# Optimization experiments

Hardware: AMD Instinct MI355X
Metric: run time of the kernel (lower is better)

Reference implementation:

```python
import jax, jax.numpy as jnp
import numpy as np

T, B = 100, 256
NUM_IN, NUM_HID, NUM_OUT = 784, 512, 10
BETA = 0.95
THRESH = 1.0   # snntorch Leaky default threshold
SLOPE = 25.0   # surrogate.fast_sigmoid default slope

# Heaviside spike with fast_sigmoid surrogate gradient (snntorch semantics)
@jax.custom_vjp
def spike_fn(x):
    return (x > 0).astype(x.dtype)

def _spike_fwd(x):
    return spike_fn(x), x

def _spike_bwd(x, g):
    return (g / (SLOPE * jnp.abs(x) + 1.0) ** 2,)

spike_fn.defvjp(_spike_fwd, _spike_bwd)

def setup_inputs() -> dict:
    key = jax.random.key(0)
    ks = jax.random.split(key, 5)
    x = jax.random.normal(ks[0], (T, B, NUM_IN), dtype=jnp.float32)
    w1 = jax.random.normal(ks[1], (NUM_HID, NUM_IN), dtype=jnp.float32) / np.float32(np.sqrt(NUM_IN))
    b1 = jax.random.normal(ks[2], (NUM_HID,), dtype=jnp.float32) * 0.01
    w2 = jax.random.normal(ks[3], (NUM_OUT, NUM_HID), dtype=jnp.float32) / np.float32(np.sqrt(NUM_HID))
    b2 = jax.random.normal(ks[4], (NUM_OUT,), dtype=jnp.float32) * 0.01
    return {"x": x, "w1": w1, "b1": b1, "w2": w2, "b2": b2}

def _snn_forward(x, w1, b1, w2, b2):
    mem1_0 = jnp.zeros((B, NUM_HID), x.dtype)
    mem2_0 = jnp.zeros((B, NUM_OUT), x.dtype)

    def step(carry, xt):
        mem1, mem2 = carry
        # layer 1: Linear + Leaky (reset-by-subtraction, reset detached as in snntorch)
        cur1 = xt @ w1.T + b1
        reset1 = jax.lax.stop_gradient(spike_fn(mem1 - THRESH))
        mem1 = BETA * mem1 + cur1 - reset1 * THRESH
        spk1 = spike_fn(mem1 - THRESH)
        # layer 2
        cur2 = spk1 @ w2.T + b2
        reset2 = jax.lax.stop_gradient(spike_fn(mem2 - THRESH))
        mem2 = BETA * mem2 + cur2 - reset2 * THRESH
        spk2 = spike_fn(mem2 - THRESH)
        return (mem1, mem2), (cur2, spk2, spk1, mem2, mem1)

    _, ys = jax.lax.scan(step, (mem1_0, mem2_0), x)
    # ys = (cur_list, spk_list, spk_hidden_list, mem_list, mem_hidden_list), stacked over T
    return ys

def reference(x, w1, b1, w2, b2):
    return _snn_forward(x, w1, b1, w2, b2)
```

## Files before the change

### kernel.cpp

```cpp
#include <hip/hip_runtime.h>
#include <stdint.h>

#define T_STEPS 100
#define BATCH   256
#define NIN     784
#define NHID    512
#define NOUT    10


#define BM 128
#define BN 128
#define BK 8
#define PANEL_K 384

__global__ __launch_bounds__(256) void gemm1_dual(
    const float* __restrict__ X, const float* __restrict__ W,
    float* __restrict__ C1, float* __restrict__ C2)
{
    __shared__ float As[2][BK][BM + 4];
    __shared__ float Bs[2][BK][BN + 4];

    const int tid = threadIdx.x;
    const int bm  = blockIdx.x * BM;
    const int bn  = blockIdx.y * BN;
    const int kb  = blockIdx.z ? PANEL_K : 0;
    float* __restrict__ C = blockIdx.z ? C2 : C1;

    const int row  = tid >> 1;
    const int koff = (tid & 1) * 4;

    const int w    = tid >> 6;
    const int lane = tid & 63;
    const int tm   = (w & 1) * 64 + (lane & 7) * 8;
    const int tn   = (w >> 1) * 64 + (lane >> 3) * 8;

    float acc[8][8];
    #pragma unroll
    for (int i = 0; i < 8; ++i)
        #pragma unroll
        for (int j = 0; j < 8; ++j) acc[i][j] = 0.f;

    const float* Xp = X + (size_t)(bm + row) * NIN + kb + koff;
    const float* Wp = W + (size_t)(bn + row) * NIN + kb + koff;

    float4 pa = *(const float4*)(Xp);
    float4 pb = *(const float4*)(Wp);
    As[0][koff+0][row] = pa.x; As[0][koff+1][row] = pa.y;
    As[0][koff+2][row] = pa.z; As[0][koff+3][row] = pa.w;
    Bs[0][koff+0][row] = pb.x; Bs[0][koff+1][row] = pb.y;
    Bs[0][koff+2][row] = pb.z; Bs[0][koff+3][row] = pb.w;

    const int NITER = PANEL_K / BK;
    for (int it = 0; it < NITER; ++it) {
        const int cur = it & 1;
        __syncthreads();

        if (it + 1 < NITER) {
            const int k0 = (it + 1) * BK;
            pa = *(const float4*)(Xp + k0);
            pb = *(const float4*)(Wp + k0);
        }

        #pragma unroll
        for (int kk = 0; kk < BK; ++kk) {
            float4 av0 = *(const float4*)&As[cur][kk][tm];
            float4 av1 = *(const float4*)&As[cur][kk][tm + 4];
            float4 bv0 = *(const float4*)&Bs[cur][kk][tn];
            float4 bv1 = *(const float4*)&Bs[cur][kk][tn + 4];
            float a[8] = {av0.x, av0.y, av0.z, av0.w, av1.x, av1.y, av1.z, av1.w};
            float b[8] = {bv0.x, bv0.y, bv0.z, bv0.w, bv1.x, bv1.y, bv1.z, bv1.w};
            #pragma unroll
            for (int i = 0; i < 8; ++i)
                #pragma unroll
                for (int j = 0; j < 8; ++j)
                    acc[i][j] = fmaf(a[i], b[j], acc[i][j]);
        }

        if (it + 1 < NITER) {
            const int nxt = cur ^ 1;
            As[nxt][koff+0][row] = pa.x; As[nxt][koff+1][row] = pa.y;
            As[nxt][koff+2][row] = pa.z; As[nxt][koff+3][row] = pa.w;
            Bs[nxt][koff+0][row] = pb.x; Bs[nxt][koff+1][row] = pb.y;
            Bs[nxt][koff+2][row] = pb.z; Bs[nxt][koff+3][row] = pb.w;
        }
    }

    #pragma unroll
    for (int i = 0; i < 8; ++i) {
        size_t r = (size_t)(bm + tm + i) * NHID + bn + tn;
        *(float4*)&C[r]     = make_float4(acc[i][0], acc[i][1], acc[i][2], acc[i][3]);
        *(float4*)&C[r + 4] = make_float4(acc[i][4], acc[i][5], acc[i][6], acc[i][7]);
    }
}

__global__ __launch_bounds__(1024) void leaky_hidden_fused(
    float* __restrict__ mem_io,
    const float* c2,
    float* spk_out,
    const float* __restrict__ X,
    const float* __restrict__ W1,
    const float* __restrict__ b1)
{
    __shared__ float4 xs4[T_STEPS][4];
    __shared__ float  p1s[2][8][NHID];
    __shared__ float  p2s[2][8][NHID];

    const int tid = threadIdx.x;
    const int bb  = blockIdx.x;
    const size_t STRIDE = (size_t)BATCH * NHID;
    const size_t base   = (size_t)bb * NHID;

    if (tid < T_STEPS * 4) {
        const int t = tid >> 2, q = tid & 3;
        xs4[t][q] = *(const float4*)(X + (size_t)t * BATCH * NIN
                                       + (size_t)bb * NIN + 768 + q * 4);
    }

    const bool producer = (tid >= 512);
    const int  lane     = tid & 511;
    const size_t col    = base + lane;

    float wt[16];
    float bias = 0.f;
    float mem  = 0.f;

    if (producer) {
        float v1[8], v2[8];
        #pragma unroll
        for (int j = 0; j < 8; ++j) {
            v1[j] = mem_io[col + (size_t)j * STRIDE];
            v2[j] = c2[col + (size_t)j * STRIDE];
        }
        #pragma unroll
        for (int j = 0; j < 8; ++j) {
            p1s[0][j][lane] = v1[j];
            p2s[0][j][lane] = v2[j];
        }
    } else {
        const int h = lane;
        const float* wp = W1 + (size_t)h * NIN + 768;
        float4 w0  = *(const float4*)(wp);
        float4 w1v = *(const float4*)(wp + 4);
        float4 w2v = *(const float4*)(wp + 8);
        float4 w3v = *(const float4*)(wp + 12);
        wt[0]=w0.x;  wt[1]=w0.y;  wt[2]=w0.z;  wt[3]=w0.w;
        wt[4]=w1v.x; wt[5]=w1v.y; wt[6]=w1v.z; wt[7]=w1v.w;
        wt[8]=w2v.x; wt[9]=w2v.y; wt[10]=w2v.z; wt[11]=w2v.w;
        wt[12]=w3v.x; wt[13]=w3v.y; wt[14]=w3v.z; wt[15]=w3v.w;
        bias = b1[h];
    }

    __syncthreads();

    for (int c = 0; c <= 12; ++c) {
        if (producer) {
            if (c < 12) {
                const int t0 = (c + 1) * 8;
                const int nb = (c + 1 == 12) ? 4 : 8;
                float v1[8], v2[8];
                #pragma unroll
                for (int j = 0; j < 8; ++j) {
                    if (j < nb) {
                        v1[j] = mem_io[col + (size_t)(t0 + j) * STRIDE];
                        v2[j] = c2[col + (size_t)(t0 + j) * STRIDE];
                    }
                }
                const int pb = (c + 1) & 1;
                #pragma unroll
                for (int j = 0; j < 8; ++j) {
                    if (j < nb) {
                        p1s[pb][j][lane] = v1[j];
                        p2s[pb][j][lane] = v2[j];
                    }
                }
            }
        } else {
            const int nt = (c == 12) ? 4 : 8;
            const int cb = c & 1;
            #pragma unroll
            for (int j = 0; j < 8; ++j) {
                if (j < nt) {
                    const int t = c * 8 + j;
                    const float p1 = p1s[cb][j][lane];
                    const float p2 = p2s[cb][j][lane];
                    float4 v0 = xs4[t][0], v1 = xs4[t][1];
                    float4 v2 = xs4[t][2], v3 = xs4[t][3];
                    float a = 0.f;
                    a = fmaf(v0.x, wt[0], a);  a = fmaf(v0.y, wt[1], a);
                    a = fmaf(v0.z, wt[2], a);  a = fmaf(v0.w, wt[3], a);
                    a = fmaf(v1.x, wt[4], a);  a = fmaf(v1.y, wt[5], a);
                    a = fmaf(v1.z, wt[6], a);  a = fmaf(v1.w, wt[7], a);
                    a = fmaf(v2.x, wt[8], a);  a = fmaf(v2.y, wt[9], a);
                    a = fmaf(v2.z, wt[10], a); a = fmaf(v2.w, wt[11], a);
                    a = fmaf(v3.x, wt[12], a); a = fmaf(v3.y, wt[13], a);
                    a = fmaf(v3.z, wt[14], a); a = fmaf(v3.w, wt[15], a);

                    const float cur = __fadd_rn(__fadd_rn(__fadd_rn(p1, p2), a), bias);
                    const float rst = (mem > 1.0f) ? 1.0f : 0.0f;
                    mem = __fsub_rn(__fadd_rn(__fmul_rn(0.95f, mem), cur), rst);

                    const size_t off = col + (size_t)t * STRIDE;
                    spk_out[off] = (mem > 1.0f) ? 1.0f : 0.0f;
                    mem_io[off]  = mem;
                }
            }
        }
        __syncthreads();
    }
}

#define G2_ROWS 32
#define W2PAD  (NHID + 4)

__global__ __launch_bounds__(320) void gemm2_f64(
    const float* __restrict__ spk1, const float* __restrict__ W2,
    const float* __restrict__ b2, float* __restrict__ cur2)
{
    __shared__ float w2s[NOUT][W2PAD];
    const int tid = threadIdx.x;
    for (int i = tid; i < NOUT * NHID; i += 320)
        w2s[i >> 9][i & 511] = W2[i];
    __syncthreads();

    const int r = tid / NOUT;
    const int o = tid % NOUT;
    const size_t m = (size_t)blockIdx.x * G2_ROWS + r;
    const float* rowp = spk1 + m * NHID;
    const float* wp   = &w2s[o][0];
    double dot = 0.0;
    #pragma unroll 4
    for (int k = 0; k < NHID; k += 4) {
        float4 s  = *(const float4*)(rowp + k);
        float4 wv = *(const float4*)(wp + k);
        dot = fma((double)s.x, (double)wv.x, dot);
        dot = fma((double)s.y, (double)wv.y, dot);
        dot = fma((double)s.z, (double)wv.z, dot);
        dot = fma((double)s.w, (double)wv.w, dot);
    }
    cur2[m * NOUT + o] = (float)(dot + (double)b2[o]);
}

__global__ __launch_bounds__(256) void leaky_out_kernel(
    const float* __restrict__ cur2, float* __restrict__ spk2,
    float* __restrict__ mem2)
{
    const int idx = blockIdx.x * blockDim.x + threadIdx.x;
    if (idx >= BATCH * NOUT) return;
    const int STRIDE = BATCH * NOUT;

    float cur[T_STEPS];
    #pragma unroll
    for (int t = 0; t < T_STEPS; ++t)
        cur[t] = cur2[(size_t)t * STRIDE + idx];

    float mem = 0.f;
    #pragma unroll
    for (int t = 0; t < T_STEPS; ++t) {
        const float rst = (mem > 1.0f) ? 1.0f : 0.0f;
        mem = __fsub_rn(__fadd_rn(__fmul_rn(0.95f, mem), cur[t]), rst);
        const size_t off = (size_t)t * STRIDE + idx;
        spk2[off] = (mem > 1.0f) ? 1.0f : 0.0f;
        mem2[off] = mem;
    }
}

extern "C" void kernel_launch(void* const* d_in, const int* in_sizes, int n_in,
                              void* d_out, int out_size, void* d_ws, size_t ws_size,
                              hipStream_t stream) {
    const float* x  = (const float*)d_in[0];
    const float* w1 = (const float*)d_in[1];
    const float* b1 = (const float*)d_in[2];
    const float* w2 = (const float*)d_in[3];
    const float* b2 = (const float*)d_in[4];

    float* out = (float*)d_out;
    float* cur2_out = out;
    float* spk2_out = out + 256000;
    float* spk1_out = out + 512000;
    float* mem2_out = out + 13619200;
    float* mem1_out = out + 13875200;

    const int M = T_STEPS * BATCH;

    const size_t p2_bytes = (size_t)M * NHID * sizeof(float);
    float* p2buf = (d_ws != nullptr && ws_size >= p2_bytes)
                       ? (float*)d_ws : spk1_out;

    dim3 gp(M / BM, NHID / BN, 2);
    gemm1_dual<<<gp, 256, 0, stream>>>(x, w1, mem1_out, p2buf);

    leaky_hidden_fused<<<BATCH, 1024, 0, stream>>>(
        mem1_out, p2buf, spk1_out, x, w1, b1);

    gemm2_f64<<<M / G2_ROWS, 320, 0, stream>>>(spk1_out, w2, b2, cur2_out);

    leaky_out_kernel<<<(BATCH * NOUT + 255) / 256, 256, 0, stream>>>(
        cur2_out, spk2_out, mem2_out);
}
```

Before: 444.2 us.

## Fuse output-layer GEMM and leaky recurrence into one per-batch kernel

Replaces the separate fp64-accumulated output GEMM and output leaky-integration kernels with a single kernel, one block per batch row. W2 is kept in registers, each wave computes one timestep's 10 outputs with a two-stage LDS reduction, and the 100-step membrane recurrence runs from shared memory. This removes a kernel launch and the reload of cur2 from global memory. In exchange, the recurrence runs on only 10 threads per block, and intra-wave LDS syncs rely on waitcnt rather than barriers.

Result: no change. 437.0 us (-1.6%).

```diff
diff --git a/kernel.cpp b/kernel.cpp
--- a/kernel.cpp
+++ b/kernel.cpp
@@ -209,58 +209,79 @@
     }
 }
 
-#define G2_ROWS 32
-#define W2PAD  (NHID + 4)
-
-__global__ __launch_bounds__(320) void gemm2_f64(
+__global__ __launch_bounds__(512) void gemm2_lout_fused(
     const float* __restrict__ spk1, const float* __restrict__ W2,
-    const float* __restrict__ b2, float* __restrict__ cur2)
+    const float* __restrict__ b2, float* __restrict__ cur2,
+    float* __restrict__ spk2, float* __restrict__ mem2)
 {
-    __shared__ float w2s[NOUT][W2PAD];
-    const int tid = threadIdx.x;
-    for (int i = tid; i < NOUT * NHID; i += 320)
-        w2s[i >> 9][i & 511] = W2[i];
+    __shared__ double ps [8][64][10];
+    __shared__ double ps2[8][4][10];
+    __shared__ float  c2s[T_STEPS][10];
+
+    const int tid  = threadIdx.x;
+    const int w    = tid >> 6;
+    const int lane = tid & 63;
+    const int b    = blockIdx.x;
+
+    float w2r[10][8];
+    #pragma unroll
+    for (int o = 0; o < NOUT; ++o) {
+        float4 a0 = *(const float4*)(W2 + (size_t)o * NHID + 8 * lane);
+        float4 a1 = *(const float4*)(W2 + (size_t)o * NHID + 8 * lane + 4);
+        w2r[o][0]=a0.x; w2r[o][1]=a0.y; w2r[o][2]=a0.z; w2r[o][3]=a0.w;
+        w2r[o][4]=a1.x; w2r[o][5]=a1.y; w2r[o][6]=a1.z; w2r[o][7]=a1.w;
+    }
+
+    for (int t = w; t < T_STEPS; t += 8) {
+        const float* sp = spk1 + (size_t)t * (BATCH * NHID)
+                               + (size_t)b * NHID + 8 * lane;
+        float4 s0 = *(const float4*)(sp);
+        float4 s1 = *(const float4*)(sp + 4);
+        const float s[8] = {s0.x, s0.y, s0.z, s0.w, s1.x, s1.y, s1.z, s1.w};
+
+        #pragma unroll
+        for (int o = 0; o < NOUT; ++o) {
+            double d = 0.0;
+            #pragma unroll
+            for (int j = 0; j < 8; ++j)
+                d = fma((double)s[j], (double)w2r[o][j], d);
+            ps[w][lane][o] = d;
+        }
+        __builtin_amdgcn_s_waitcnt(0);
+
+        if (lane < 40) {
+            const int o = lane >> 2, g = lane & 3;
+            double d = 0.0;
+            #pragma unroll
+            for (int l2 = 0; l2 < 16; ++l2)
+                d += ps[w][g * 16 + l2][o];
+            ps2[w][g][o] = d;
+        }
+        __builtin_amdgcn_s_waitcnt(0);
+
+        if (lane < 10) {
+            const int o = lane;
+            double d = ((ps2[w][0][o] + ps2[w][1][o]) + ps2[w][2][o])
+                       + ps2[w][3][o];
+            const float c = (float)(d + (double)b2[o]);
+            cur2[(size_t)t * (BATCH * NOUT) + (size_t)b * NOUT + o] = c;
+            c2s[t][o] = c;
+        }
+    }
+
     __syncthreads();
 
-    const int r = tid / NOUT;
-    const int o = tid % NOUT;
-    const size_t m = (size_t)blockIdx.x * G2_ROWS + r;
-    const float* rowp = spk1 + m * NHID;
-    const float* wp   = &w2s[o][0];
-    double dot = 0.0;
-    #pragma unroll 4
-    for (int k = 0; k < NHID; k += 4) {
-        float4 s  = *(const float4*)(rowp + k);
-        float4 wv = *(const float4*)(wp + k);
-        dot = fma((double)s.x, (double)wv.x, dot);
-        dot = fma((double)s.y, (double)wv.y, dot);
-        dot = fma((double)s.z, (double)wv.z, dot);
-        dot = fma((double)s.w, (double)wv.w, dot);
-    }
-    cur2[m * NOUT + o] = (float)(dot + (double)b2[o]);
-}
-
-__global__ __launch_bounds__(256) void leaky_out_kernel(
-    const float* __restrict__ cur2, float* __restrict__ spk2,
-    float* __restrict__ mem2)
-{
-    const int idx = blockIdx.x * blockDim.x + threadIdx.x;
-    if (idx >= BATCH * NOUT) return;
-    const int STRIDE = BATCH * NOUT;
-
-    float cur[T_STEPS];
-    #pragma unroll
-    for (int t = 0; t < T_STEPS; ++t)
-        cur[t] = cur2[(size_t)t * STRIDE + idx];
-
-    float mem = 0.f;
-    #pragma unroll
-    for (int t = 0; t < T_STEPS; ++t) {
-        const float rst = (mem > 1.0f) ? 1.0f : 0.0f;
-        mem = __fsub_rn(__fadd_rn(__fmul_rn(0.95f, mem), cur[t]), rst);
-        const size_t off = (size_t)t * STRIDE + idx;
-        spk2[off] = (mem > 1.0f) ? 1.0f : 0.0f;
-        mem2[off] = mem;
+    if (tid < NOUT) {
+        const int o = tid;
+        float mem = 0.f;
+        for (int t = 0; t < T_STEPS; ++t) {
+            const float cur = c2s[t][o];
+            const float rst = (mem > 1.0f) ? 1.0f : 0.0f;
+            mem = __fsub_rn(__fadd_rn(__fmul_rn(0.95f, mem), cur), rst);
+            const size_t off = (size_t)t * (BATCH * NOUT) + (size_t)b * NOUT + o;
+            spk2[off] = (mem > 1.0f) ? 1.0f : 0.0f;
+            mem2[off] = mem;
+        }
     }
 }
 
@@ -292,8 +313,6 @@
     leaky_hidden_fused<<<BATCH, 1024, 0, stream>>>(
         mem1_out, p2buf, spk1_out, x, w1, b1);
 
-    gemm2_f64<<<M / G2_ROWS, 320, 0, stream>>>(spk1_out, w2, b2, cur2_out);
-
-    leaky_out_kernel<<<(BATCH * NOUT + 255) / 256, 256, 0, stream>>>(
-        cur2_out, spk2_out, mem2_out);
+    gemm2_lout_fused<<<BATCH, 512, 0, stream>>>(
+        spk1_out, w2, b2, cur2_out, spk2_out, mem2_out);
 }
```
